# Kernel tuning notes

Measured on AMD Instinct MI355X. Metric: run time of the kernel, lower is better.

## Reference

```python
import jax, jax.numpy as jnp
import numpy as np


def setup_inputs() -> dict:
    key = jax.random.key(0)
    B, T, C = 8, 4096, 768
    k1, k2, k3, k4 = jax.random.split(key, 4)
    # Per-channel time-decay (w) and time-first (u) weights; real RWKV uses
    # negative decay but the log-domain max-subtraction math is stable either way.
    w = jax.random.normal(k1, (C,), dtype=jnp.float32)
    u = jax.random.normal(k2, (C,), dtype=jnp.float32)
    k = jax.random.normal(k3, (B, T, C), dtype=jnp.float32)
    v = jax.random.normal(k4, (B, T, C), dtype=jnp.float32)
    return {"B": B, "T": T, "C": C, "w": w, "u": u, "k": k, "v": v}


def reference(B, T, C, w, u, k, v):
    # Faithful JAX port of wkv_pytorch: numerically-stable log-domain RWKV
    # WKV recurrence, vectorized over (B, C) and scanned over T.
    NEG_INF = -1e38
    wf = w.astype(jnp.float32)
    uf = u.astype(jnp.float32)
    kf = k.astype(jnp.float32)
    vf = v.astype(jnp.float32)

    def step(carry, inp):
        aa, bb, pp = carry           # each (B, C)
        kt, vt = inp                 # each (B, C)
        ww = uf + kt                 # u broadcast over batch
        p = jnp.maximum(pp, ww)
        e1 = jnp.exp(pp - p)
        e2 = jnp.exp(ww - p)
        yt = (e1 * aa + e2 * vt) / (e1 * bb + e2)
        ww2 = wf + pp
        p2 = jnp.maximum(ww2, kt)
        e1b = jnp.exp(ww2 - p2)
        e2b = jnp.exp(kt - p2)
        return (e1b * aa + e2b * vt, e1b * bb + e2b, p2), yt

    Bn, Cn = kf.shape[0], kf.shape[2]
    init = (
        jnp.zeros((Bn, Cn), jnp.float32),
        jnp.zeros((Bn, Cn), jnp.float32),
        jnp.full((Bn, Cn), NEG_INF, jnp.float32),
    )
    kT = jnp.swapaxes(kf, 0, 1)  # (T, B, C) for scan over time
    vT = jnp.swapaxes(vf, 0, 1)
    _, y = jax.lax.scan(step, init, (kT, vT))
    y = jnp.swapaxes(y, 0, 1)    # back to (B, T, C)
    return y.astype(k.dtype)
```

## Files before the change

kernel.cpp:

```cpp
#include <hip/hip_runtime.h>
#include <math.h>


#define NEG_INF (-1e38f)
#define GSZ 4

__device__ __forceinline__ void wkv_step(float& aa, float& bb, float& pp,
                                         float wc, float kt, float vt) {
    float ww = wc + pp;
    float p  = fmaxf(ww, kt);
    float d  = ww - kt;
    float e  = __expf(-fabsf(d));
    float e1 = (d >= 0.f) ? 1.f : e;
    float e2 = (d >= 0.f) ? e   : 1.f;
    aa = e1 * aa + e2 * vt;
    bb = e1 * bb + e2;
    pp = p;
}

__device__ __forceinline__ float wkv_ostep(float aa, float bb, float pp,
                                           float uc, float kt, float vt) {
    float ww = uc + kt;
    float d  = pp - ww;
    float e  = __expf(-fabsf(d));
    float e1 = (d >= 0.f) ? 1.f : e;
    float e2 = (d >= 0.f) ? e   : 1.f;
    return __fdividef(e1 * aa + e2 * vt, e1 * bb + e2);
}

__global__ __launch_bounds__(384, 6)
void wkv_chunk_state(const float* __restrict__ w,
                     const float* __restrict__ kg,
                     const float* __restrict__ vg,
                     float* __restrict__ sa,
                     float* __restrict__ sb,
                     float* __restrict__ sp,
                     int B, int T, int C, int L, int NC) {
    const int bj  = blockIdx.x;
    const int b   = bj / NC;
    const int j   = bj - b * NC;
    const int tid = threadIdx.x;
    const int C2  = C >> 1;

    const float2* kp = (const float2*)(kg + ((size_t)b * T + (size_t)j * L) * C) + tid;
    const float2* vp = (const float2*)(vg + ((size_t)b * T + (size_t)j * L) * C) + tid;
    const float2  wc = ((const float2*)w)[tid];

    float aa0 = 0.f, bb0 = 0.f, pp0 = NEG_INF;
    float aa1 = 0.f, bb1 = 0.f, pp1 = NEG_INF;

    float2 kb[GSZ], vb[GSZ];
    #pragma unroll
    for (int g = 0; g < GSZ; ++g) { kb[g] = kp[g * C2]; vb[g] = vp[g * C2]; }

    for (int t0 = 0; t0 < L - GSZ; t0 += GSZ) {
        float2 kn[GSZ], vn[GSZ];
        #pragma unroll
        for (int g = 0; g < GSZ; ++g) {
            kn[g] = kp[(t0 + GSZ + g) * C2];
            vn[g] = vp[(t0 + GSZ + g) * C2];
        }
        #pragma unroll
        for (int g = 0; g < GSZ; ++g) {
            wkv_step(aa0, bb0, pp0, wc.x, kb[g].x, vb[g].x);
            wkv_step(aa1, bb1, pp1, wc.y, kb[g].y, vb[g].y);
        }
        #pragma unroll
        for (int g = 0; g < GSZ; ++g) { kb[g] = kn[g]; vb[g] = vn[g]; }
    }
    #pragma unroll
    for (int g = 0; g < GSZ; ++g) {
        wkv_step(aa0, bb0, pp0, wc.x, kb[g].x, vb[g].x);
        wkv_step(aa1, bb1, pp1, wc.y, kb[g].y, vb[g].y);
    }

    const int base = j * (B * C) + b * C + 2 * tid;
    *(float2*)(sa + base) = make_float2(aa0, aa1);
    *(float2*)(sb + base) = make_float2(bb0, bb1);
    *(float2*)(sp + base) = make_float2(pp0, pp1);
}

__global__ void wkv_prefix(const float* __restrict__ w,
                           float* __restrict__ sa,
                           float* __restrict__ sb,
                           float* __restrict__ sp,
                           int B, int C, int L, int NC) {
    int bc = blockIdx.x * blockDim.x + threadIdx.x;
    int BC = B * C;
    if (bc >= BC) return;
    int c = bc % C;
    float wL = w[c] * (float)L;

    float aa = 0.f, bb = 0.f, pp = NEG_INF;
    for (int j = 0; j < NC; ++j) {
        int idx = j * BC + bc;
        float la = sa[idx];
        float lb = sb[idx];
        float lp = sp[idx];
        sa[idx] = aa; sb[idx] = bb; sp[idx] = pp;
        float ppd = pp + wL;
        float p   = fmaxf(ppd, lp);
        float e1  = __expf(ppd - p);
        float e2  = __expf(lp - p);
        aa = e1 * aa + e2 * la;
        bb = e1 * bb + e2 * lb;
        pp = p;
    }
}

__global__ __launch_bounds__(384, 6)
void wkv_out(const float* __restrict__ w,
             const float* __restrict__ u,
             const float* __restrict__ kg,
             const float* __restrict__ vg,
             const float* __restrict__ sa,
             const float* __restrict__ sb,
             const float* __restrict__ sp,
             float* __restrict__ y,
             int B, int T, int C, int L, int NC) {
    const int bj  = blockIdx.x;
    const int b   = bj / NC;
    const int j   = bj - b * NC;
    const int tid = threadIdx.x;
    const int C2  = C >> 1;

    const size_t rowbase = ((size_t)b * T + (size_t)j * L) * C;
    const float2* kp = (const float2*)(kg + rowbase) + tid;
    const float2* vp = (const float2*)(vg + rowbase) + tid;
    float2*       yp = (float2*)(y + rowbase) + tid;
    const float2  wc = ((const float2*)w)[tid];
    const float2  uc = ((const float2*)u)[tid];

    const int base = j * (B * C) + b * C + 2 * tid;
    float2 a2 = *(const float2*)(sa + base);
    float2 b2 = *(const float2*)(sb + base);
    float2 p2 = *(const float2*)(sp + base);
    float aa0 = a2.x, bb0 = b2.x, pp0 = p2.x;
    float aa1 = a2.y, bb1 = b2.y, pp1 = p2.y;

    float2 kb[GSZ], vb[GSZ];
    #pragma unroll
    for (int g = 0; g < GSZ; ++g) { kb[g] = kp[g * C2]; vb[g] = vp[g * C2]; }

    for (int t0 = 0; t0 < L - GSZ; t0 += GSZ) {
        float2 kn[GSZ], vn[GSZ];
        #pragma unroll
        for (int g = 0; g < GSZ; ++g) {
            kn[g] = kp[(t0 + GSZ + g) * C2];
            vn[g] = vp[(t0 + GSZ + g) * C2];
        }
        #pragma unroll
        for (int g = 0; g < GSZ; ++g) {
            float2 yo;
            yo.x = wkv_ostep(aa0, bb0, pp0, uc.x, kb[g].x, vb[g].x);
            yo.y = wkv_ostep(aa1, bb1, pp1, uc.y, kb[g].y, vb[g].y);
            yp[(t0 + g) * C2] = yo;
            wkv_step(aa0, bb0, pp0, wc.x, kb[g].x, vb[g].x);
            wkv_step(aa1, bb1, pp1, wc.y, kb[g].y, vb[g].y);
        }
        #pragma unroll
        for (int g = 0; g < GSZ; ++g) { kb[g] = kn[g]; vb[g] = vn[g]; }
    }
    const int tl = L - GSZ;
    #pragma unroll
    for (int g = 0; g < GSZ; ++g) {
        float2 yo;
        yo.x = wkv_ostep(aa0, bb0, pp0, uc.x, kb[g].x, vb[g].x);
        yo.y = wkv_ostep(aa1, bb1, pp1, uc.y, kb[g].y, vb[g].y);
        yp[(tl + g) * C2] = yo;
        wkv_step(aa0, bb0, pp0, wc.x, kb[g].x, vb[g].x);
        wkv_step(aa1, bb1, pp1, wc.y, kb[g].y, vb[g].y);
    }
}

extern "C" void kernel_launch(void* const* d_in, const int* in_sizes, int n_in,
                              void* d_out, int out_size, void* d_ws, size_t ws_size,
                              hipStream_t stream) {
    const float* w = (const float*)d_in[3];
    const float* u = (const float*)d_in[4];
    const float* k = (const float*)d_in[5];
    const float* v = (const float*)d_in[6];
    float* y = (float*)d_out;

    const int C  = in_sizes[3];
    const int BT = in_sizes[5] / C;
    const int T  = 4096;
    const int B  = BT / T;

    int NC = 128;
    while (NC > 1 && ((size_t)3 * B * C * NC * sizeof(float) > ws_size ||
                      (T % NC) != 0 || ((T / NC) % GSZ) != 0))
        NC >>= 1;
    const int L = T / NC;

    const int BC    = B * C;
    const int total = BC * NC;
    float* sa = (float*)d_ws;
    float* sb = sa + total;
    float* sp = sb + total;

    const int nblk = B * NC;
    const int bthr = C / 2;

    wkv_chunk_state<<<nblk, bthr, 0, stream>>>(w, k, v, sa, sb, sp, B, T, C, L, NC);
    wkv_prefix<<<(BC + 255) / 256, 256, 0, stream>>>(w, sa, sb, sp, B, C, L, NC);
    wkv_out<<<nblk, bthr, 0, stream>>>(w, u, k, v, sa, sb, sp, y, B, T, C, L, NC);
}
```

Baseline: 125.2 us.

## Use 256 chunks with two-level parallel prefix scan and float4 vectorized passes

Raises the chunk count to 256 with 16 timesteps per chunk. The serial prefix over chunk states is replaced by a two-level scan: a local scan within groups of 16 chunks, then a scan over group totals. The output pass combines the group carry with the local inclusive prefix. It also widens per-thread work to float4 with 192-thread blocks, preloads the whole chunk into registers, and uses nontemporal stores for y. The aim is to shorten the serial prefix phase and raise memory-level parallelism, at the cost of an extra launch, more scratch memory, and higher register pressure.

New measurement: 104.2 us (median of 3 runs). 16.7% less time.

```diff
diff --git a/kernel.cpp b/kernel.cpp
--- a/kernel.cpp
+++ b/kernel.cpp
@@ -3,7 +3,12 @@
 
 
 #define NEG_INF (-1e38f)
-#define GSZ 4
+#define NCC 256
+#define SCW 16
+#define NSC (NCC / SCW)
+#define LL  16
+
+typedef float f4 __attribute__((ext_vector_type(4)));
 
 __device__ __forceinline__ void wkv_step(float& aa, float& bb, float& pp,
                                          float wc, float kt, float vt) {
@@ -28,148 +33,169 @@
     return __fdividef(e1 * aa + e2 * vt, e1 * bb + e2);
 }
 
-__global__ __launch_bounds__(384, 6)
-void wkv_chunk_state(const float* __restrict__ w,
-                     const float* __restrict__ kg,
-                     const float* __restrict__ vg,
-                     float* __restrict__ sa,
-                     float* __restrict__ sb,
-                     float* __restrict__ sp,
-                     int B, int T, int C, int L, int NC) {
-    const int bj  = blockIdx.x;
-    const int b   = bj / NC;
-    const int j   = bj - b * NC;
+__device__ __forceinline__ void wkv_combine(float& aa, float& bb, float& pp,
+                                            float dw, float la, float lb, float lp) {
+    float ppd = pp + dw;
+    float p   = fmaxf(ppd, lp);
+    float e1  = __expf(ppd - p);
+    float e2  = __expf(lp - p);
+    aa = e1 * aa + e2 * la;
+    bb = e1 * bb + e2 * lb;
+    pp = p;
+}
+
+__global__ __launch_bounds__(192)
+void wkv_pass1(const float* __restrict__ w,
+               const float* __restrict__ kg,
+               const float* __restrict__ vg,
+               float* __restrict__ sa, float* __restrict__ sb,
+               float* __restrict__ sp,
+               int B, int T, int C) {
+    const int b   = blockIdx.x / NCC;
+    const int j   = blockIdx.x % NCC;
     const int tid = threadIdx.x;
-    const int C2  = C >> 1;
-
-    const float2* kp = (const float2*)(kg + ((size_t)b * T + (size_t)j * L) * C) + tid;
-    const float2* vp = (const float2*)(vg + ((size_t)b * T + (size_t)j * L) * C) + tid;
-    const float2  wc = ((const float2*)w)[tid];
-
-    float aa0 = 0.f, bb0 = 0.f, pp0 = NEG_INF;
-    float aa1 = 0.f, bb1 = 0.f, pp1 = NEG_INF;
-
-    float2 kb[GSZ], vb[GSZ];
-    #pragma unroll
-    for (int g = 0; g < GSZ; ++g) { kb[g] = kp[g * C2]; vb[g] = vp[g * C2]; }
-
-    for (int t0 = 0; t0 < L - GSZ; t0 += GSZ) {
-        float2 kn[GSZ], vn[GSZ];
-        #pragma unroll
-        for (int g = 0; g < GSZ; ++g) {
-            kn[g] = kp[(t0 + GSZ + g) * C2];
-            vn[g] = vp[(t0 + GSZ + g) * C2];
+    const int C4  = C >> 2;
+
+    const f4* kp = (const f4*)(kg + ((size_t)b * T + (size_t)j * LL) * C) + tid;
+    const f4* vp = (const f4*)(vg + ((size_t)b * T + (size_t)j * LL) * C) + tid;
+    const f4  wc = ((const f4*)w)[tid];
+
+    f4 kb[LL], vb[LL];
+    #pragma unroll
+    for (int t = 0; t < LL; ++t) { kb[t] = kp[t * C4]; vb[t] = vp[t * C4]; }
+    __builtin_amdgcn_sched_group_barrier(0x20, 2 * LL + 1, 0);
+
+    float aa[4] = {0.f, 0.f, 0.f, 0.f};
+    float bb[4] = {0.f, 0.f, 0.f, 0.f};
+    float pp[4] = {NEG_INF, NEG_INF, NEG_INF, NEG_INF};
+    #pragma unroll
+    for (int t = 0; t < LL; ++t) {
+        #pragma unroll
+        for (int q = 0; q < 4; ++q) {
+            float kt = kb[t][q], vt = vb[t][q];
+            wkv_step(aa[q], bb[q], pp[q], wc[q], kt, vt);
         }
-        #pragma unroll
-        for (int g = 0; g < GSZ; ++g) {
-            wkv_step(aa0, bb0, pp0, wc.x, kb[g].x, vb[g].x);
-            wkv_step(aa1, bb1, pp1, wc.y, kb[g].y, vb[g].y);
+    }
+
+    const int base = j * (B * C) + b * C;
+    f4 oa = {aa[0], aa[1], aa[2], aa[3]};
+    f4 ob = {bb[0], bb[1], bb[2], bb[3]};
+    f4 op = {pp[0], pp[1], pp[2], pp[3]};
+    ((f4*)(sa + base))[tid] = oa;
+    ((f4*)(sb + base))[tid] = ob;
+    ((f4*)(sp + base))[tid] = op;
+}
+
+__global__ void wkv_scan_local(const float* __restrict__ w,
+                               float* __restrict__ sa, float* __restrict__ sb,
+                               float* __restrict__ sp,
+                               int B, int C) {
+    const int BC = B * C;
+    int tid = blockIdx.x * blockDim.x + threadIdx.x;
+    if (tid >= BC * NSC) return;
+    const int bc = tid % BC;
+    const int sc = tid / BC;
+    const float wL = w[bc % C] * (float)LL;
+
+    float la[SCW], lb[SCW], lp[SCW];
+    #pragma unroll
+    for (int i = 0; i < SCW; ++i) {
+        const int idx = (sc * SCW + i) * BC + bc;
+        la[i] = sa[idx]; lb[i] = sb[idx]; lp[i] = sp[idx];
+    }
+    float aa = 0.f, bb = 0.f, pp = NEG_INF;
+    #pragma unroll
+    for (int i = 0; i < SCW; ++i) {
+        wkv_combine(aa, bb, pp, wL, la[i], lb[i], lp[i]);
+        const int idx = (sc * SCW + i) * BC + bc;
+        sa[idx] = aa; sb[idx] = bb; sp[idx] = pp;
+    }
+}
+
+__global__ void wkv_scan_super(const float* __restrict__ w,
+                               float* __restrict__ sa, float* __restrict__ sb,
+                               float* __restrict__ sp,
+                               int B, int C) {
+    const int BC = B * C;
+    int bc = blockIdx.x * blockDim.x + threadIdx.x;
+    if (bc >= BC) return;
+    const float wSL = w[bc % C] * (float)(LL * SCW);
+
+    float ta[NSC], tb[NSC], tp[NSC];
+    #pragma unroll
+    for (int sc = 0; sc < NSC; ++sc) {
+        const int idx = (sc * SCW + (SCW - 1)) * BC + bc;
+        ta[sc] = sa[idx]; tb[sc] = sb[idx]; tp[sc] = sp[idx];
+    }
+    float aa = 0.f, bb = 0.f, pp = NEG_INF;
+    #pragma unroll
+    for (int sc = 0; sc < NSC; ++sc) {
+        const int idx = (sc * SCW + (SCW - 1)) * BC + bc;
+        sa[idx] = aa; sb[idx] = bb; sp[idx] = pp;
+        wkv_combine(aa, bb, pp, wSL, ta[sc], tb[sc], tp[sc]);
+    }
+}
+
+__global__ __launch_bounds__(192)
+void wkv_pass3(const float* __restrict__ w, const float* __restrict__ u,
+               const float* __restrict__ kg, const float* __restrict__ vg,
+               const float* __restrict__ sa, const float* __restrict__ sb,
+               const float* __restrict__ sp,
+               float* __restrict__ y,
+               int B, int T, int C) {
+    const int b   = blockIdx.x / NCC;
+    const int j   = blockIdx.x % NCC;
+    const int tid = threadIdx.x;
+    const int C4  = C >> 2;
+    const int BC  = B * C;
+
+    const size_t rowbase = ((size_t)b * T + (size_t)j * LL) * C;
+    const f4* kp = (const f4*)(kg + rowbase) + tid;
+    const f4* vp = (const f4*)(vg + rowbase) + tid;
+    f4*       yp = (f4*)(y + rowbase) + tid;
+    const f4  wc = ((const f4*)w)[tid];
+    const f4  uc = ((const f4*)u)[tid];
+
+    f4 kb[LL], vb[LL];
+    #pragma unroll
+    for (int t = 0; t < LL; ++t) { kb[t] = kp[t * C4]; vb[t] = vp[t * C4]; }
+    __builtin_amdgcn_sched_group_barrier(0x20, 2 * LL, 0);
+
+    const int sc = j / SCW;
+    const int i  = j % SCW;
+    const int slot_last = (sc * SCW + (SCW - 1)) * BC + b * C;
+    f4 Ea = ((const f4*)(sa + slot_last))[tid];
+    f4 Eb = ((const f4*)(sb + slot_last))[tid];
+    f4 Ep = ((const f4*)(sp + slot_last))[tid];
+
+    float aa[4], bb[4], pp[4];
+    if (i == 0) {
+        #pragma unroll
+        for (int q = 0; q < 4; ++q) { aa[q] = Ea[q]; bb[q] = Eb[q]; pp[q] = Ep[q]; }
+    } else {
+        const int prev = (j - 1) * BC + b * C;
+        f4 la = ((const f4*)(sa + prev))[tid];
+        f4 lb = ((const f4*)(sb + prev))[tid];
+        f4 lp = ((const f4*)(sp + prev))[tid];
+        const float steps = (float)(i * LL);
+        #pragma unroll
+        for (int q = 0; q < 4; ++q) {
+            float a = Ea[q], bq = Eb[q], p = Ep[q];
+            wkv_combine(a, bq, p, wc[q] * steps, la[q], lb[q], lp[q]);
+            aa[q] = a; bb[q] = bq; pp[q] = p;
         }
-        #pragma unroll
-        for (int g = 0; g < GSZ; ++g) { kb[g] = kn[g]; vb[g] = vn[g]; }
-    }
-    #pragma unroll
-    for (int g = 0; g < GSZ; ++g) {
-        wkv_step(aa0, bb0, pp0, wc.x, kb[g].x, vb[g].x);
-        wkv_step(aa1, bb1, pp1, wc.y, kb[g].y, vb[g].y);
-    }
-
-    const int base = j * (B * C) + b * C + 2 * tid;
-    *(float2*)(sa + base) = make_float2(aa0, aa1);
-    *(float2*)(sb + base) = make_float2(bb0, bb1);
-    *(float2*)(sp + base) = make_float2(pp0, pp1);
-}
-
-__global__ void wkv_prefix(const float* __restrict__ w,
-                           float* __restrict__ sa,
-                           float* __restrict__ sb,
-                           float* __restrict__ sp,
-                           int B, int C, int L, int NC) {
-    int bc = blockIdx.x * blockDim.x + threadIdx.x;
-    int BC = B * C;
-    if (bc >= BC) return;
-    int c = bc % C;
-    float wL = w[c] * (float)L;
-
-    float aa = 0.f, bb = 0.f, pp = NEG_INF;
-    for (int j = 0; j < NC; ++j) {
-        int idx = j * BC + bc;
-        float la = sa[idx];
-        float lb = sb[idx];
-        float lp = sp[idx];
-        sa[idx] = aa; sb[idx] = bb; sp[idx] = pp;
-        float ppd = pp + wL;
-        float p   = fmaxf(ppd, lp);
-        float e1  = __expf(ppd - p);
-        float e2  = __expf(lp - p);
-        aa = e1 * aa + e2 * la;
-        bb = e1 * bb + e2 * lb;
-        pp = p;
-    }
-}
-
-__global__ __launch_bounds__(384, 6)
-void wkv_out(const float* __restrict__ w,
-             const float* __restrict__ u,
-             const float* __restrict__ kg,
-             const float* __restrict__ vg,
-             const float* __restrict__ sa,
-             const float* __restrict__ sb,
-             const float* __restrict__ sp,
-             float* __restrict__ y,
-             int B, int T, int C, int L, int NC) {
-    const int bj  = blockIdx.x;
-    const int b   = bj / NC;
-    const int j   = bj - b * NC;
-    const int tid = threadIdx.x;
-    const int C2  = C >> 1;
-
-    const size_t rowbase = ((size_t)b * T + (size_t)j * L) * C;
-    const float2* kp = (const float2*)(kg + rowbase) + tid;
-    const float2* vp = (const float2*)(vg + rowbase) + tid;
-    float2*       yp = (float2*)(y + rowbase) + tid;
-    const float2  wc = ((const float2*)w)[tid];
-    const float2  uc = ((const float2*)u)[tid];
-
-    const int base = j * (B * C) + b * C + 2 * tid;
-    float2 a2 = *(const float2*)(sa + base);
-    float2 b2 = *(const float2*)(sb + base);
-    float2 p2 = *(const float2*)(sp + base);
-    float aa0 = a2.x, bb0 = b2.x, pp0 = p2.x;
-    float aa1 = a2.y, bb1 = b2.y, pp1 = p2.y;
-
-    float2 kb[GSZ], vb[GSZ];
-    #pragma unroll
-    for (int g = 0; g < GSZ; ++g) { kb[g] = kp[g * C2]; vb[g] = vp[g * C2]; }
-
-    for (int t0 = 0; t0 < L - GSZ; t0 += GSZ) {
-        float2 kn[GSZ], vn[GSZ];
-        #pragma unroll
-        for (int g = 0; g < GSZ; ++g) {
-            kn[g] = kp[(t0 + GSZ + g) * C2];
-            vn[g] = vp[(t0 + GSZ + g) * C2];
+    }
+
+    #pragma unroll
+    for (int t = 0; t < LL; ++t) {
+        f4 yo;
+        #pragma unroll
+        for (int q = 0; q < 4; ++q) {
+            float kt = kb[t][q], vt = vb[t][q];
+            yo[q] = wkv_ostep(aa[q], bb[q], pp[q], uc[q], kt, vt);
+            wkv_step(aa[q], bb[q], pp[q], wc[q], kt, vt);
         }
-        #pragma unroll
-        for (int g = 0; g < GSZ; ++g) {
-            float2 yo;
-            yo.x = wkv_ostep(aa0, bb0, pp0, uc.x, kb[g].x, vb[g].x);
-            yo.y = wkv_ostep(aa1, bb1, pp1, uc.y, kb[g].y, vb[g].y);
-            yp[(t0 + g) * C2] = yo;
-            wkv_step(aa0, bb0, pp0, wc.x, kb[g].x, vb[g].x);
-            wkv_step(aa1, bb1, pp1, wc.y, kb[g].y, vb[g].y);
-        }
-        #pragma unroll
-        for (int g = 0; g < GSZ; ++g) { kb[g] = kn[g]; vb[g] = vn[g]; }
-    }
-    const int tl = L - GSZ;
-    #pragma unroll
-    for (int g = 0; g < GSZ; ++g) {
-        float2 yo;
-        yo.x = wkv_ostep(aa0, bb0, pp0, uc.x, kb[g].x, vb[g].x);
-        yo.y = wkv_ostep(aa1, bb1, pp1, uc.y, kb[g].y, vb[g].y);
-        yp[(tl + g) * C2] = yo;
-        wkv_step(aa0, bb0, pp0, wc.x, kb[g].x, vb[g].x);
-        wkv_step(aa1, bb1, pp1, wc.y, kb[g].y, vb[g].y);
+        __builtin_nontemporal_store(yo, yp + t * C4);
     }
 }
 
@@ -187,22 +213,17 @@
     const int T  = 4096;
     const int B  = BT / T;
 
-    int NC = 128;
-    while (NC > 1 && ((size_t)3 * B * C * NC * sizeof(float) > ws_size ||
-                      (T % NC) != 0 || ((T / NC) % GSZ) != 0))
-        NC >>= 1;
-    const int L = T / NC;
-
-    const int BC    = B * C;
-    const int total = BC * NC;
+    const int BC = B * C;
+    const size_t total = (size_t)BC * NCC;
     float* sa = (float*)d_ws;
     float* sb = sa + total;
     float* sp = sb + total;
 
-    const int nblk = B * NC;
-    const int bthr = C / 2;
-
-    wkv_chunk_state<<<nblk, bthr, 0, stream>>>(w, k, v, sa, sb, sp, B, T, C, L, NC);
-    wkv_prefix<<<(BC + 255) / 256, 256, 0, stream>>>(w, sa, sb, sp, B, C, L, NC);
-    wkv_out<<<nblk, bthr, 0, stream>>>(w, u, k, v, sa, sb, sp, y, B, T, C, L, NC);
-}
+    wkv_pass1<<<B * NCC, C / 4, 0, stream>>>(w, k, v, sa, sb, sp, B, T, C);
+
+    const int n2 = BC * NSC;
+    wkv_scan_local<<<(n2 + 255) / 256, 256, 0, stream>>>(w, sa, sb, sp, B, C);
+    wkv_scan_super<<<(BC + 255) / 256, 256, 0, stream>>>(w, sa, sb, sp, B, C);
+
+    wkv_pass3<<<B * NCC, C / 4, 0, stream>>>(w, u, k, v, sa, sb, sp, y, B, T, C);
+}
```
